# Kernel tuning notes

Hardware: AMD Instinct MI355X
Metric: run time of the kernel (lower is better)

Reference implementation:

```python
import jax, jax.numpy as jnp
import numpy as np

N_HEADS = 16
N_KV_HEADS = 4
N_EMBED = 2048
HEAD_DIM = 128
SECTIONS = [16, 24, 24, 16, 24, 24]


def _process_rotary(c):
    # c: [3, B, T, HEAD_DIM] -> [B, 1, T, HEAD_DIM]
    splits = np.cumsum(SECTIONS)[:-1]
    secs = jnp.split(c, splits, axis=-1)
    out = jnp.concatenate([s[i % 3] for i, s in enumerate(secs)], axis=-1)
    return out[:, None]  # add head axis


def _rotate_half(x):
    x1, x2 = jnp.split(x, 2, axis=-1)
    return jnp.concatenate([-x2, x1], axis=-1)


def setup_inputs() -> dict:
    key = jax.random.key(0)
    ks = jax.random.split(key, 12)
    B, T = 1, 2048
    s = 0.02
    return {
        "x": jax.random.normal(ks[0], (B, T, N_EMBED), jnp.float32),
        "cos": jax.random.uniform(ks[1], (3, B, T, HEAD_DIM), jnp.float32),
        "sin": jax.random.uniform(ks[2], (3, B, T, HEAD_DIM), jnp.float32),
        "Wq": jax.random.normal(ks[3], (N_EMBED, N_EMBED), jnp.float32) * s,
        "bq": jax.random.normal(ks[4], (N_EMBED,), jnp.float32) * s,
        "Wk": jax.random.normal(ks[5], (N_EMBED, N_KV_HEADS * HEAD_DIM), jnp.float32) * s,
        "bk": jax.random.normal(ks[6], (N_KV_HEADS * HEAD_DIM,), jnp.float32) * s,
        "Wv": jax.random.normal(ks[7], (N_EMBED, N_KV_HEADS * HEAD_DIM), jnp.float32) * s,
        "bv": jax.random.normal(ks[8], (N_KV_HEADS * HEAD_DIM,), jnp.float32) * s,
        "Wo": jax.random.normal(ks[9], (N_EMBED, N_EMBED), jnp.float32) * s,
    }


def reference(x, cos, sin, Wq, bq, Wk, bk, Wv, bv, Wo):
    B, T, C = x.shape
    H, Hkv, D = N_HEADS, N_KV_HEADS, HEAD_DIM
    q = (x @ Wq + bq).reshape(B, T, H, D).transpose(0, 2, 1, 3)    # [B,H,T,D]
    k = (x @ Wk + bk).reshape(B, T, Hkv, D).transpose(0, 2, 1, 3)  # [B,Hkv,T,D]
    v = (x @ Wv + bv).reshape(B, T, Hkv, D).transpose(0, 2, 1, 3)
    # multi-section rope (cos/sin are 4-dim -> custom path)
    c = _process_rotary(cos)
    s = _process_rotary(sin)
    q = q * c + _rotate_half(q) * s
    k = k * c + _rotate_half(k) * s
    present_k, present_v = k, v
    # GQA expansion (repeat_interleave over head axis)
    r = H // Hkv
    k = jnp.repeat(k, r, axis=1)
    v = jnp.repeat(v, r, axis=1)
    # causal SDPA
    scores = jnp.einsum("bhqd,bhkd->bhqk", q, k) / jnp.sqrt(jnp.float32(D))
    causal = jnp.tril(jnp.ones((T, T), dtype=bool))
    scores = jnp.where(causal, scores, jnp.finfo(scores.dtype).min)
    attn = jax.nn.softmax(scores, axis=-1)
    y = jnp.einsum("bhqk,bhkd->bhqd", attn, v)
    y = y.transpose(0, 2, 1, 3).reshape(B, T, C)
    y = y @ Wo
    return (y, present_k, present_v)
```

## Files before the change

kernel.cpp:

```cpp
#include <hip/hip_runtime.h>

typedef unsigned short u16;
typedef unsigned int u32;
typedef __attribute__((ext_vector_type(4))) float f32x4;
typedef __attribute__((ext_vector_type(8))) __bf16 bf16x8;
typedef __attribute__((ext_vector_type(4))) u16 u16x4;
typedef __attribute__((ext_vector_type(2))) u32 u32x2;


__device__ __forceinline__ u16 f2bf(float f) {
  union { float f; unsigned u; } v; v.f = f;
  unsigned r = v.u + 0x7fffu + ((v.u >> 16) & 1u);
  return (u16)(r >> 16);
}

__device__ __forceinline__ u32 pack_bf2(float a, float b) {
  union { float f; unsigned u; } x, y;
  x.f = a; y.f = b;
#if __has_builtin(__builtin_amdgcn_perm)
  return __builtin_amdgcn_perm(y.u + 0x8000u, x.u + 0x8000u, 0x07060302u);
#else
  return (u32)((x.u + 0x8000u) >> 16) | ((y.u + 0x8000u) & 0xffff0000u);
#endif
}

__device__ __forceinline__ void stage16(const void* g, void* l) {
#if __has_builtin(__builtin_amdgcn_global_load_lds)
  __builtin_amdgcn_global_load_lds((const __attribute__((address_space(1))) void*)g,
                                   (__attribute__((address_space(3))) void*)l, 16, 0, 0);
#else
  *(f32x4*)l = *(const f32x4*)g;
#endif
}

__device__ __forceinline__ f32x4 mfma16(bf16x8 a, bf16x8 b, f32x4 c) {
  return __builtin_amdgcn_mfma_f32_16x16x32_bf16(a, b, c, 0, 0, 0);
}

__device__ __forceinline__ float fexp2(float x) {
#if __has_builtin(__builtin_amdgcn_exp2f)
  return __builtin_amdgcn_exp2f(x);
#else
  return exp2f(x);
#endif
}

__device__ __forceinline__ int rope_ch(int d) {
  int dd = (d < 64) ? d : d - 64;
  return (dd < 16) ? 0 : (dd < 40 ? 1 : 2);
}


__global__ void yuna_convert_bf16(const float* __restrict__ in, u16* __restrict__ out, int n4) {
  int i = blockIdx.x * blockDim.x + threadIdx.x;
  if (i < n4) {
    f32x4 v = ((const f32x4*)in)[i];
    u16x4 o;
    o.x = f2bf(v.x); o.y = f2bf(v.y); o.z = f2bf(v.z); o.w = f2bf(v.w);
    ((u16x4*)out)[i] = o;
  }
}

__global__ void yuna_prep_weights(const float* __restrict__ Wq, const float* __restrict__ Wk,
                                  const float* __restrict__ Wv, const float* __restrict__ Wo,
                                  u16* __restrict__ Wb, u16* __restrict__ Wob) {
  __shared__ float tile[64][65];
  const int mat = blockIdx.z;
  const float* W;
  u16* out;
  int N;
  if (mat == 0)      { W = Wq; out = Wb;                          N = 2048; }
  else if (mat == 1) { W = Wk; out = Wb + (size_t)2048 * 2048;    N = 512; }
  else if (mat == 2) { W = Wv; out = Wb + (size_t)2560 * 2048;    N = 512; }
  else               { W = Wo; out = Wob;                         N = 2048; }
  int k0 = blockIdx.x * 64, n0 = blockIdx.y * 64;
  if (n0 >= N) return;
  int tx = threadIdx.x & 63, ty = threadIdx.x >> 6;
#pragma unroll
  for (int j = 0; j < 64; j += 4)
    tile[ty + j][tx] = W[(size_t)(k0 + ty + j) * N + n0 + tx];
  __syncthreads();
#pragma unroll
  for (int j = 0; j < 64; j += 4)
    out[(size_t)(n0 + ty + j) * 2048 + k0 + tx] = f2bf(tile[tx][ty + j]);
}

__global__ void yuna_transpose_v(const float* __restrict__ pv, u16* __restrict__ vtb) {
  __shared__ float tile[64][65];
  int t0 = blockIdx.x * 64, d0 = blockIdx.y * 64, kvh = blockIdx.z;
  int tx = threadIdx.x & 63, ty = threadIdx.x >> 6;
#pragma unroll
  for (int j = 0; j < 64; j += 4)
    tile[ty + j][tx] = pv[(size_t)(kvh * 2048 + t0 + ty + j) * 128 + d0 + tx];
  __syncthreads();
#pragma unroll
  for (int j = 0; j < 64; j += 4)
    vtb[(size_t)(kvh * 128 + d0 + ty + j) * 2048 + t0 + tx] = f2bf(tile[tx][ty + j]);
}

template <int WN>
__global__ __launch_bounds__(256, 2) void yuna_gemm_bt(
    const u16* __restrict__ A, const u16* __restrict__ Bt,
    float* __restrict__ C, int M, int N, int K) {
  constexpr int NF = WN / 16;
  constexpr int BROWS = 2 * WN;
  __shared__ __align__(16) u16 As[128 * 64];
  __shared__ __align__(16) u16 Bs[BROWS * 64];
  const int tid = threadIdx.x;
  const int wave = tid >> 6, lane = tid & 63;
  const int m0 = blockIdx.x * 128, n0 = blockIdx.y * (2 * WN);
  const int wr = (wave >> 1) * 64, wc = (wave & 1) * WN;
  const int lrow = lane & 15, lkg = lane >> 4;

  const int srow = tid >> 3;
  const int ssc = (tid & 7) ^ ((tid >> 3) & 7);
  const size_t abase = (size_t)(m0 + srow) * K + ssc * 8;
  const size_t bbase = (size_t)(n0 + srow) * K + ssc * 8;

  const f32x4 fzero = {0.f, 0.f, 0.f, 0.f};
  f32x4 acc[4][NF];
#pragma unroll
  for (int mi = 0; mi < 4; ++mi)
#pragma unroll
    for (int ni = 0; ni < NF; ++ni) acc[mi][ni] = fzero;

  const int sw = lrow & 7;
  for (int k0 = 0; k0 < K; k0 += 64) {
    __syncthreads();
#pragma unroll
    for (int it = 0; it < 4; ++it)
      stage16(A + abase + (size_t)it * 32 * K + k0, (char*)As + (tid + it * 256) * 16);
#pragma unroll
    for (int it = 0; it < BROWS / 32; ++it)
      stage16(Bt + bbase + (size_t)it * 32 * K + k0, (char*)Bs + (tid + it * 256) * 16);
    asm volatile("s_waitcnt vmcnt(0)" ::: "memory");
    __syncthreads();
#pragma unroll
    for (int kk = 0; kk < 2; ++kk) {
      const int cof = ((kk * 4 + lkg) ^ sw) << 4;
      bf16x8 af[4], bfr[NF];
#pragma unroll
      for (int mi = 0; mi < 4; ++mi)
        af[mi] = *(const bf16x8*)((const char*)As + (wr + mi * 16 + lrow) * 128 + cof);
#pragma unroll
      for (int ni = 0; ni < NF; ++ni)
        bfr[ni] = *(const bf16x8*)((const char*)Bs + (wc + ni * 16 + lrow) * 128 + cof);
#pragma unroll
      for (int mi = 0; mi < 4; ++mi)
#pragma unroll
        for (int ni = 0; ni < NF; ++ni)
          acc[mi][ni] = mfma16(af[mi], bfr[ni], acc[mi][ni]);
    }
  }
#pragma unroll
  for (int mi = 0; mi < 4; ++mi)
#pragma unroll
    for (int ni = 0; ni < NF; ++ni) {
      int r0 = m0 + wr + mi * 16 + lkg * 4;
      int c = n0 + wc + ni * 16 + lrow;
#pragma unroll
      for (int r = 0; r < 4; ++r)
        C[(size_t)(r0 + r) * N + c] = acc[mi][ni][r];
    }
}

__global__ void yuna_rope_scatter(
    const float* __restrict__ qkv, const float* __restrict__ bq,
    const float* __restrict__ bk, const float* __restrict__ bv,
    const float* __restrict__ cosp, const float* __restrict__ sinp,
    u16* __restrict__ qb, u16* __restrict__ kb,
    float* __restrict__ pk, float* __restrict__ pv) {
  const float QSCALE = 1.4426950408889634f * 0.08838834764831845f;
  int t = blockIdx.x;
  int tid = threadIdx.x;
  const float* row = qkv + (size_t)t * 3072;
  size_t cbase = (size_t)t * 128;
  for (int i = tid; i < 1024; i += 256) {
    int h = i >> 6, d = i & 63;
    float a = row[h * 128 + d] + bq[h * 128 + d];
    float b = row[h * 128 + d + 64] + bq[h * 128 + d + 64];
    float c0 = cosp[(size_t)rope_ch(d) * 262144 + cbase + d];
    float s0 = sinp[(size_t)rope_ch(d) * 262144 + cbase + d];
    float c1 = cosp[(size_t)rope_ch(d + 64) * 262144 + cbase + d + 64];
    float s1 = sinp[(size_t)rope_ch(d + 64) * 262144 + cbase + d + 64];
    float o0 = a * c0 - b * s0;
    float o1 = b * c1 + a * s1;
    size_t o = ((size_t)h * 2048 + t) * 128 + d;
    qb[o] = f2bf(o0 * QSCALE);
    qb[o + 64] = f2bf(o1 * QSCALE);
  }
  {
    int kvh = tid >> 6, d = tid & 63;
    float a = row[2048 + kvh * 128 + d] + bk[kvh * 128 + d];
    float b = row[2048 + kvh * 128 + d + 64] + bk[kvh * 128 + d + 64];
    float c0 = cosp[(size_t)rope_ch(d) * 262144 + cbase + d];
    float s0 = sinp[(size_t)rope_ch(d) * 262144 + cbase + d];
    float c1 = cosp[(size_t)rope_ch(d + 64) * 262144 + cbase + d + 64];
    float s1 = sinp[(size_t)rope_ch(d + 64) * 262144 + cbase + d + 64];
    float o0 = a * c0 - b * s0;
    float o1 = b * c1 + a * s1;
    size_t o = ((size_t)kvh * 2048 + t) * 128 + d;
    kb[o] = f2bf(o0); kb[o + 64] = f2bf(o1);
    pk[o] = o0; pk[o + 64] = o1;
  }
  for (int i = tid; i < 512; i += 256) {
    int kvh = i >> 7, d = i & 127;
    pv[((size_t)kvh * 2048 + t) * 128 + d] = row[2560 + kvh * 128 + d] + bv[kvh * 128 + d];
  }
}

__global__ __launch_bounds__(256, 2) void yuna_flash_attn(
    const u16* __restrict__ Q,
    const u16* __restrict__ Kb,
    const u16* __restrict__ Vt,
    u16* __restrict__ Y) {
  __shared__ __align__(16) u16 Ks[2][64 * 128];
  __shared__ __align__(16) u16 Vs[2][128 * 64];
  __shared__ __align__(16) u16 Ps[64 * 64];
  const int h = blockIdx.x;
  const int yb = blockIdx.y;
  const int qb = (yb < 16) ? yb : 47 - yb;
  const int kvh = h >> 2;
  const int tid = threadIdx.x, wave = tid >> 6, lane = tid & 63;
  const int lrow = lane & 15, lkg = lane >> 4;
  const int m = wave * 16 + lrow;
  const int sw = lrow & 7;

  const int krow = tid >> 4;
  const int ksc = (tid & 15) ^ ((tid >> 4) & 7);
  const size_t kbase0 = ((size_t)(kvh * 2048 + krow) << 7) + ksc * 8;
  const int vrow = tid >> 3;
  const int vsc = (tid & 7) ^ ((tid >> 3) & 7);
  const size_t vbase0 = (size_t)(kvh * 128 + vrow) * 2048 + vsc * 8;

  bf16x8 qf[4];
#pragma unroll
  for (int kk = 0; kk < 4; ++kk)
    qf[kk] = *(const bf16x8*)(Q + (((size_t)h * 2048 + qb * 64 + m) << 7) + kk * 32 + lkg * 8);

  const f32x4 fzero = {0.f, 0.f, 0.f, 0.f};
  f32x4 o[8];
#pragma unroll
  for (int dt = 0; dt < 8; ++dt) o[dt] = fzero;
  float m_i = -1e30f, l_i = 0.f;

  const int nkb = qb + 1;

#pragma unroll
  for (int it = 0; it < 4; ++it)
    stage16(Kb + kbase0 + ((size_t)(it * 16) << 7), (char*)Ks[0] + (tid + it * 256) * 16);
#pragma unroll
  for (int it = 0; it < 4; ++it)
    stage16(Vt + vbase0 + (size_t)it * 32 * 2048, (char*)Vs[0] + (tid + it * 256) * 16);

  for (int kb = 0; kb < nkb; ++kb) {
    const int cur = kb & 1;
    const char* Ksb = (const char*)Ks[cur];
    const char* Vsb = (const char*)Vs[cur];
    if (kb + 1 < nkb) {
      char* Ksn = (char*)Ks[cur ^ 1];
      char* Vsn = (char*)Vs[cur ^ 1];
#pragma unroll
      for (int it = 0; it < 4; ++it)
        stage16(Kb + kbase0 + ((size_t)((kb + 1) * 64 + it * 16) << 7), Ksn + (tid + it * 256) * 16);
#pragma unroll
      for (int it = 0; it < 4; ++it)
        stage16(Vt + vbase0 + (size_t)it * 32 * 2048 + (kb + 1) * 64, Vsn + (tid + it * 256) * 16);
      asm volatile("s_waitcnt vmcnt(8)\n\ts_barrier" ::: "memory");
    } else {
      asm volatile("s_waitcnt vmcnt(0)\n\ts_barrier" ::: "memory");
    }

    f32x4 s[4];
#pragma unroll
    for (int nt = 0; nt < 4; ++nt) s[nt] = fzero;
#pragma unroll
    for (int kk = 0; kk < 4; ++kk) {
      const int cof = ((kk * 4 + lkg) ^ sw) << 4;
      bf16x8 kf[4];
#pragma unroll
      for (int nt = 0; nt < 4; ++nt)
        kf[nt] = *(const bf16x8*)(Ksb + (nt * 16 + lrow) * 256 + cof);
#pragma unroll
      for (int nt = 0; nt < 4; ++nt)
        s[nt] = mfma16(kf[nt], qf[kk], s[nt]);
    }
    if (kb == qb) {
#pragma unroll
      for (int nt = 0; nt < 4; ++nt)
#pragma unroll
        for (int r = 0; r < 4; ++r)
          if (nt * 16 + lkg * 4 + r > m) s[nt][r] = -1e30f;
    }

    float mx = -1e30f;
#pragma unroll
    for (int nt = 0; nt < 4; ++nt)
#pragma unroll
      for (int r = 0; r < 4; ++r) mx = fmaxf(mx, s[nt][r]);
    mx = fmaxf(mx, __shfl_xor(mx, 16));
    mx = fmaxf(mx, __shfl_xor(mx, 32));
    float mnew = fmaxf(m_i, mx);
    float alpha = fexp2(m_i - mnew);
    m_i = mnew;
    float ps = 0.f;
    const int hh = lkg & 1;
#pragma unroll
    for (int nt = 0; nt < 4; ++nt) {
      float p0 = fexp2(s[nt][0] - mnew);
      float p1 = fexp2(s[nt][1] - mnew);
      float p2 = fexp2(s[nt][2] - mnew);
      float p3 = fexp2(s[nt][3] - mnew);
      ps += (p0 + p1) + (p2 + p3);
      u32x2 pk2;
      pk2.x = pack_bf2(p0, p1);
      pk2.y = pack_bf2(p2, p3);
      int cc = 2 * nt + (lkg >> 1);
      *(u32x2*)((char*)Ps + m * 128 + ((cc ^ (m & 7)) << 4) + hh * 8) = pk2;
    }
    ps += __shfl_xor(ps, 16);
    ps += __shfl_xor(ps, 32);
    l_i = l_i * alpha + ps;
#pragma unroll
    for (int dt = 0; dt < 8; ++dt) o[dt] *= alpha;

#pragma unroll
    for (int kk = 0; kk < 2; ++kk) {
      const int cof = ((kk * 4 + lkg) ^ sw) << 4;
      bf16x8 pf = *(const bf16x8*)((char*)Ps + m * 128 + cof);
      bf16x8 vf[8];
#pragma unroll
      for (int dt = 0; dt < 8; ++dt)
        vf[dt] = *(const bf16x8*)(Vsb + (dt * 16 + lrow) * 128 + cof);
#pragma unroll
      for (int dt = 0; dt < 8; ++dt)
        o[dt] = mfma16(vf[dt], pf, o[dt]);
    }
    asm volatile("s_barrier" ::: "memory");
  }

  __syncthreads();
  {
    float inv = 1.f / l_i;
    const int hh = lkg & 1;
#pragma unroll
    for (int dt = 0; dt < 8; ++dt) {
      u32x2 w2;
      w2.x = pack_bf2(o[dt][0] * inv, o[dt][1] * inv);
      w2.y = pack_bf2(o[dt][2] * inv, o[dt][3] * inv);
      int cc = 2 * dt + (lkg >> 1);
      *(u32x2*)((char*)Ks[0] + m * 256 + ((cc ^ (m & 7)) << 4) + hh * 8) = w2;
    }
  }
  __syncthreads();
#pragma unroll
  for (int it = 0; it < 4; ++it) {
    int c = tid + it * 256;
    int row = c >> 4, cc = c & 15;
    f32x4 v = *(const f32x4*)((const char*)Ks[0] + row * 256 + ((cc ^ (row & 7)) << 4));
    *(f32x4*)(Y + (size_t)(qb * 64 + row) * 2048 + h * 128 + cc * 8) = v;
  }
}


extern "C" void kernel_launch(void* const* d_in, const int* in_sizes, int n_in,
                              void* d_out, int out_size, void* d_ws, size_t ws_size,
                              hipStream_t stream) {
  const float* x = (const float*)d_in[0];
  const float* cosp = (const float*)d_in[1];
  const float* sinp = (const float*)d_in[2];
  const float* Wq = (const float*)d_in[3];
  const float* bq = (const float*)d_in[4];
  const float* Wk = (const float*)d_in[5];
  const float* bk = (const float*)d_in[6];
  const float* Wv = (const float*)d_in[7];
  const float* bv = (const float*)d_in[8];
  const float* Wo = (const float*)d_in[9];
  float* out = (float*)d_out;
  float* out_k = out + 4194304;
  float* out_v = out + 5242880;

  char* ws = (char*)d_ws;
  u16* xb   = (u16*)(ws + 0);
  u16* Wb   = (u16*)(ws + 8388608);
  u16* Wob  = (u16*)(ws + 20971520);
  float* qkv = (float*)(ws + 29360128);
  u16* qbuf = (u16*)(ws + 54525952);
  u16* kbuf = (u16*)(ws + 62914560);
  u16* vtb  = (u16*)(ws + 65011712);
  u16* yat  = (u16*)(ws + 67108864);

  yuna_convert_bf16<<<4096, 256, 0, stream>>>(x, xb, 1048576);
  yuna_prep_weights<<<dim3(32, 32, 4), 256, 0, stream>>>(Wq, Wk, Wv, Wo, Wb, Wob);
  yuna_gemm_bt<48><<<dim3(16, 32), 256, 0, stream>>>(xb, Wb, qkv, 2048, 3072, 2048);
  yuna_rope_scatter<<<2048, 256, 0, stream>>>(qkv, bq, bk, bv, cosp, sinp,
                                              qbuf, kbuf, out_k, out_v);
  yuna_transpose_v<<<dim3(32, 2, 4), 256, 0, stream>>>(out_v, vtb);
  yuna_flash_attn<<<dim3(16, 32), 256, 0, stream>>>(qbuf, kbuf, vtb, yat);
  yuna_gemm_bt<32><<<dim3(16, 32), 256, 0, stream>>>(yat, Wob, out, 2048, 2048, 2048);
}
```

Before: 242.2 us.

## Fuse bias, RoPE and V transpose into QKV GEMM epilogue with double-buffered tiles

The QKV GEMM now writes bf16 Q/K, the fp32 present K/V and the transposed bf16 V directly from its epilogue. It applies bias and RoPE there using cos/sin tables pre-selected per section in the convert kernel. This removes the fp32 qkv intermediate plus the separate rope_scatter and transpose_v kernels. Both GEMMs switch to 64x128 tiles with double-buffered LDS staging and occupancy 3, trading larger grids for overlap of loads with MFMA. The epilogue writes are scattered 2-byte stores, which may be less coalesced.

```diff
diff --git a/kernel.cpp b/kernel.cpp
--- a/kernel.cpp
+++ b/kernel.cpp
@@ -51,13 +51,29 @@
 }
 
 
-__global__ void yuna_convert_bf16(const float* __restrict__ in, u16* __restrict__ out, int n4) {
-  int i = blockIdx.x * blockDim.x + threadIdx.x;
-  if (i < n4) {
+__global__ void yuna_convert_prep(const float* __restrict__ in, u16* __restrict__ out,
+                                  const float* __restrict__ cosp, const float* __restrict__ sinp,
+                                  float* __restrict__ csel, float* __restrict__ ssel) {
+  int b = blockIdx.x;
+  if (b < 4096) {
+    int i = b * 256 + threadIdx.x;
     f32x4 v = ((const f32x4*)in)[i];
     u16x4 o;
     o.x = f2bf(v.x); o.y = f2bf(v.y); o.z = f2bf(v.z); o.w = f2bf(v.w);
     ((u16x4*)out)[i] = o;
+  } else {
+    int i = (b - 4096) * 256 + threadIdx.x;
+    int i4 = i * 4;
+    int t = i4 >> 7, d = i4 & 127;
+    f32x4 c, s;
+#pragma unroll
+    for (int j = 0; j < 4; ++j) {
+      int ch = rope_ch(d + j);
+      c[j] = cosp[(size_t)ch * 262144 + (size_t)t * 128 + d + j];
+      s[j] = sinp[(size_t)ch * 262144 + (size_t)t * 128 + d + j];
+    }
+    ((f32x4*)csel)[i] = c;
+    ((f32x4*)ssel)[i] = s;
   }
 }
 
@@ -85,32 +101,21 @@
     out[(size_t)(n0 + ty + j) * 2048 + k0 + tx] = f2bf(tile[tx][ty + j]);
 }
 
-__global__ void yuna_transpose_v(const float* __restrict__ pv, u16* __restrict__ vtb) {
-  __shared__ float tile[64][65];
-  int t0 = blockIdx.x * 64, d0 = blockIdx.y * 64, kvh = blockIdx.z;
-  int tx = threadIdx.x & 63, ty = threadIdx.x >> 6;
-#pragma unroll
-  for (int j = 0; j < 64; j += 4)
-    tile[ty + j][tx] = pv[(size_t)(kvh * 2048 + t0 + ty + j) * 128 + d0 + tx];
-  __syncthreads();
-#pragma unroll
-  for (int j = 0; j < 64; j += 4)
-    vtb[(size_t)(kvh * 128 + d0 + ty + j) * 2048 + t0 + tx] = f2bf(tile[tx][ty + j]);
-}
-
-template <int WN>
-__global__ __launch_bounds__(256, 2) void yuna_gemm_bt(
+__global__ __launch_bounds__(256, 3) void yuna_gemm_qkv(
     const u16* __restrict__ A, const u16* __restrict__ Bt,
-    float* __restrict__ C, int M, int N, int K) {
-  constexpr int NF = WN / 16;
-  constexpr int BROWS = 2 * WN;
-  __shared__ __align__(16) u16 As[128 * 64];
-  __shared__ __align__(16) u16 Bs[BROWS * 64];
+    const float* __restrict__ bq, const float* __restrict__ bk, const float* __restrict__ bv,
+    const float* __restrict__ csel, const float* __restrict__ ssel,
+    u16* __restrict__ qb, u16* __restrict__ kb, u16* __restrict__ vtb,
+    float* __restrict__ pk, float* __restrict__ pv) {
+  const int K = 2048;
+  __shared__ __align__(16) char smem[49152];
   const int tid = threadIdx.x;
   const int wave = tid >> 6, lane = tid & 63;
-  const int m0 = blockIdx.x * 128, n0 = blockIdx.y * (2 * WN);
-  const int wr = (wave >> 1) * 64, wc = (wave & 1) * WN;
   const int lrow = lane & 15, lkg = lane >> 4;
+  const int m0 = blockIdx.x * 64;
+  const int by = blockIdx.y;
+  const int n0 = by * 128;
+  const int sw = lrow & 7;
 
   const int srow = tid >> 3;
   const int ssc = (tid & 7) ^ ((tid >> 3) & 7);
@@ -118,95 +123,179 @@
   const size_t bbase = (size_t)(n0 + srow) * K + ssc * 8;
 
   const f32x4 fzero = {0.f, 0.f, 0.f, 0.f};
-  f32x4 acc[4][NF];
-#pragma unroll
-  for (int mi = 0; mi < 4; ++mi)
-#pragma unroll
-    for (int ni = 0; ni < NF; ++ni) acc[mi][ni] = fzero;
-
-  const int sw = lrow & 7;
-  for (int k0 = 0; k0 < K; k0 += 64) {
-    __syncthreads();
-#pragma unroll
-    for (int it = 0; it < 4; ++it)
-      stage16(A + abase + (size_t)it * 32 * K + k0, (char*)As + (tid + it * 256) * 16);
-#pragma unroll
-    for (int it = 0; it < BROWS / 32; ++it)
-      stage16(Bt + bbase + (size_t)it * 32 * K + k0, (char*)Bs + (tid + it * 256) * 16);
-    asm volatile("s_waitcnt vmcnt(0)" ::: "memory");
-    __syncthreads();
+  f32x4 acc[4][2];
+#pragma unroll
+  for (int mi = 0; mi < 4; ++mi) { acc[mi][0] = fzero; acc[mi][1] = fzero; }
+
+#pragma unroll
+  for (int it = 0; it < 2; ++it)
+    stage16(A + abase + (size_t)it * 32 * K, smem + (tid + it * 256) * 16);
+#pragma unroll
+  for (int it = 0; it < 4; ++it)
+    stage16(Bt + bbase + (size_t)it * 32 * K, smem + 16384 + (tid + it * 256) * 16);
+
+  for (int k0 = 0, ki = 0; k0 < K; k0 += 64, ++ki) {
+    const int cur = ki & 1;
+    const char* Asb = smem + cur * 8192;
+    const char* Bsb = smem + 16384 + cur * 16384;
+    if (k0 + 64 < K) {
+      char* Asn = smem + (cur ^ 1) * 8192;
+      char* Bsn = smem + 16384 + (cur ^ 1) * 16384;
+#pragma unroll
+      for (int it = 0; it < 2; ++it)
+        stage16(A + abase + (size_t)it * 32 * K + k0 + 64, Asn + (tid + it * 256) * 16);
+#pragma unroll
+      for (int it = 0; it < 4; ++it)
+        stage16(Bt + bbase + (size_t)it * 32 * K + k0 + 64, Bsn + (tid + it * 256) * 16);
+      asm volatile("s_waitcnt vmcnt(6)\n\ts_barrier" ::: "memory");
+    } else {
+      asm volatile("s_waitcnt vmcnt(0)\n\ts_barrier" ::: "memory");
+    }
 #pragma unroll
     for (int kk = 0; kk < 2; ++kk) {
       const int cof = ((kk * 4 + lkg) ^ sw) << 4;
-      bf16x8 af[4], bfr[NF];
+      bf16x8 af[4], bfr[2];
 #pragma unroll
       for (int mi = 0; mi < 4; ++mi)
-        af[mi] = *(const bf16x8*)((const char*)As + (wr + mi * 16 + lrow) * 128 + cof);
-#pragma unroll
-      for (int ni = 0; ni < NF; ++ni)
-        bfr[ni] = *(const bf16x8*)((const char*)Bs + (wc + ni * 16 + lrow) * 128 + cof);
+        af[mi] = *(const bf16x8*)(Asb + (mi * 16 + lrow) * 128 + cof);
+#pragma unroll
+      for (int ni = 0; ni < 2; ++ni)
+        bfr[ni] = *(const bf16x8*)(Bsb + (wave * 16 + ni * 64 + lrow) * 128 + cof);
 #pragma unroll
       for (int mi = 0; mi < 4; ++mi)
 #pragma unroll
-        for (int ni = 0; ni < NF; ++ni)
+        for (int ni = 0; ni < 2; ++ni)
           acc[mi][ni] = mfma16(af[mi], bfr[ni], acc[mi][ni]);
     }
+    asm volatile("s_barrier" ::: "memory");
+  }
+
+  if (by >= 20) {
+    const int kvh = by - 20;
+#pragma unroll
+    for (int mi = 0; mi < 4; ++mi)
+#pragma unroll
+      for (int ni = 0; ni < 2; ++ni) {
+        int d = wave * 16 + ni * 64 + lrow;
+        float bb = bv[kvh * 128 + d];
+        int mb = mi * 16 + lkg * 4;
+        float v0 = acc[mi][ni][0] + bb, v1 = acc[mi][ni][1] + bb;
+        float v2 = acc[mi][ni][2] + bb, v3 = acc[mi][ni][3] + bb;
+        size_t pb = ((size_t)(kvh * 2048 + m0 + mb)) * 128 + d;
+        pv[pb] = v0; pv[pb + 128] = v1; pv[pb + 256] = v2; pv[pb + 384] = v3;
+        u16x4 w;
+        w.x = f2bf(v0); w.y = f2bf(v1); w.z = f2bf(v2); w.w = f2bf(v3);
+        *(u16x4*)(vtb + ((size_t)(kvh * 128 + d)) * 2048 + m0 + mb) = w;
+      }
+  } else {
+    const float QSCALE = 1.4426950408889634f * 0.08838834764831845f;
+    const bool isQ = (by < 16);
+    const int h = isQ ? by : (by - 16);
+    const float* bias = isQ ? bq : bk;
+    const int dlo = wave * 16 + lrow;
+    const float blo = bias[h * 128 + dlo];
+    const float bhi = bias[h * 128 + dlo + 64];
+#pragma unroll
+    for (int mi = 0; mi < 4; ++mi) {
+      const int tb = m0 + mi * 16 + lkg * 4;
+#pragma unroll
+      for (int r = 0; r < 4; ++r) {
+        const int t = tb + r;
+        float a = acc[mi][0][r] + blo;
+        float b = acc[mi][1][r] + bhi;
+        size_t cb = (size_t)t * 128 + dlo;
+        float cl = csel[cb], sl = ssel[cb];
+        float ch = csel[cb + 64], sh = ssel[cb + 64];
+        float lo = a * cl - b * sl;
+        float hi = b * ch + a * sh;
+        size_t o = (((size_t)(h * 2048 + t)) << 7) + dlo;
+        if (isQ) {
+          qb[o] = f2bf(lo * QSCALE);
+          qb[o + 64] = f2bf(hi * QSCALE);
+        } else {
+          kb[o] = f2bf(lo);
+          kb[o + 64] = f2bf(hi);
+          pk[o] = lo; pk[o + 64] = hi;
+        }
+      }
+    }
+  }
+}
+
+__global__ __launch_bounds__(256, 3) void yuna_gemm_out(
+    const u16* __restrict__ A, const u16* __restrict__ Bt, float* __restrict__ C) {
+  const int K = 2048;
+  __shared__ __align__(16) char smem[49152];
+  const int tid = threadIdx.x;
+  const int wave = tid >> 6, lane = tid & 63;
+  const int lrow = lane & 15, lkg = lane >> 4;
+  const int m0 = blockIdx.x * 64;
+  const int n0 = blockIdx.y * 128;
+  const int wc = wave * 32;
+  const int sw = lrow & 7;
+
+  const int srow = tid >> 3;
+  const int ssc = (tid & 7) ^ ((tid >> 3) & 7);
+  const size_t abase = (size_t)(m0 + srow) * K + ssc * 8;
+  const size_t bbase = (size_t)(n0 + srow) * K + ssc * 8;
+
+  const f32x4 fzero = {0.f, 0.f, 0.f, 0.f};
+  f32x4 acc[4][2];
+#pragma unroll
+  for (int mi = 0; mi < 4; ++mi) { acc[mi][0] = fzero; acc[mi][1] = fzero; }
+
+#pragma unroll
+  for (int it = 0; it < 2; ++it)
+    stage16(A + abase + (size_t)it * 32 * K, smem + (tid + it * 256) * 16);
+#pragma unroll
+  for (int it = 0; it < 4; ++it)
+    stage16(Bt + bbase + (size_t)it * 32 * K, smem + 16384 + (tid + it * 256) * 16);
+
+  for (int k0 = 0, ki = 0; k0 < K; k0 += 64, ++ki) {
+    const int cur = ki & 1;
+    const char* Asb = smem + cur * 8192;
+    const char* Bsb = smem + 16384 + cur * 16384;
+    if (k0 + 64 < K) {
+      char* Asn = smem + (cur ^ 1) * 8192;
+      char* Bsn = smem + 16384 + (cur ^ 1) * 16384;
+#pragma unroll
+      for (int it = 0; it < 2; ++it)
+        stage16(A + abase + (size_t)it * 32 * K + k0 + 64, Asn + (tid + it * 256) * 16);
+#pragma unroll
+      for (int it = 0; it < 4; ++it)
+        stage16(Bt + bbase + (size_t)it * 32 * K + k0 + 64, Bsn + (tid + it * 256) * 16);
+      asm volatile("s_waitcnt vmcnt(6)\n\ts_barrier" ::: "memory");
+    } else {
+      asm volatile("s_waitcnt vmcnt(0)\n\ts_barrier" ::: "memory");
+    }
+#pragma unroll
+    for (int kk = 0; kk < 2; ++kk) {
+      const int cof = ((kk * 4 + lkg) ^ sw) << 4;
+      bf16x8 af[4], bfr[2];
+#pragma unroll
+      for (int mi = 0; mi < 4; ++mi)
+        af[mi] = *(const bf16x8*)(Asb + (mi * 16 + lrow) * 128 + cof);
+#pragma unroll
+      for (int ni = 0; ni < 2; ++ni)
+        bfr[ni] = *(const bf16x8*)(Bsb + (wc + ni * 16 + lrow) * 128 + cof);
+#pragma unroll
+      for (int mi = 0; mi < 4; ++mi)
+#pragma unroll
+        for (int ni = 0; ni < 2; ++ni)
+          acc[mi][ni] = mfma16(af[mi], bfr[ni], acc[mi][ni]);
+    }
+    asm volatile("s_barrier" ::: "memory");
   }
 #pragma unroll
   for (int mi = 0; mi < 4; ++mi)
 #pragma unroll
-    for (int ni = 0; ni < NF; ++ni) {
-      int r0 = m0 + wr + mi * 16 + lkg * 4;
-      int c = n0 + wc + ni * 16 + lrow;
+    for (int ni = 0; ni < 2; ++ni) {
+      int d = wc + ni * 16 + lrow;
+      int mb = mi * 16 + lkg * 4;
 #pragma unroll
       for (int r = 0; r < 4; ++r)
-        C[(size_t)(r0 + r) * N + c] = acc[mi][ni][r];
-    }
-}
-
-__global__ void yuna_rope_scatter(
-    const float* __restrict__ qkv, const float* __restrict__ bq,
-    const float* __restrict__ bk, const float* __restrict__ bv,
-    const float* __restrict__ cosp, const float* __restrict__ sinp,
-    u16* __restrict__ qb, u16* __restrict__ kb,
-    float* __restrict__ pk, float* __restrict__ pv) {
-  const float QSCALE = 1.4426950408889634f * 0.08838834764831845f;
-  int t = blockIdx.x;
-  int tid = threadIdx.x;
-  const float* row = qkv + (size_t)t * 3072;
-  size_t cbase = (size_t)t * 128;
-  for (int i = tid; i < 1024; i += 256) {
-    int h = i >> 6, d = i & 63;
-    float a = row[h * 128 + d] + bq[h * 128 + d];
-    float b = row[h * 128 + d + 64] + bq[h * 128 + d + 64];
-    float c0 = cosp[(size_t)rope_ch(d) * 262144 + cbase + d];
-    float s0 = sinp[(size_t)rope_ch(d) * 262144 + cbase + d];
-    float c1 = cosp[(size_t)rope_ch(d + 64) * 262144 + cbase + d + 64];
-    float s1 = sinp[(size_t)rope_ch(d + 64) * 262144 + cbase + d + 64];
-    float o0 = a * c0 - b * s0;
-    float o1 = b * c1 + a * s1;
-    size_t o = ((size_t)h * 2048 + t) * 128 + d;
-    qb[o] = f2bf(o0 * QSCALE);
-    qb[o + 64] = f2bf(o1 * QSCALE);
-  }
-  {
-    int kvh = tid >> 6, d = tid & 63;
-    float a = row[2048 + kvh * 128 + d] + bk[kvh * 128 + d];
-    float b = row[2048 + kvh * 128 + d + 64] + bk[kvh * 128 + d + 64];
-    float c0 = cosp[(size_t)rope_ch(d) * 262144 + cbase + d];
-    float s0 = sinp[(size_t)rope_ch(d) * 262144 + cbase + d];
-    float c1 = cosp[(size_t)rope_ch(d + 64) * 262144 + cbase + d + 64];
-    float s1 = sinp[(size_t)rope_ch(d + 64) * 262144 + cbase + d + 64];
-    float o0 = a * c0 - b * s0;
-    float o1 = b * c1 + a * s1;
-    size_t o = ((size_t)kvh * 2048 + t) * 128 + d;
-    kb[o] = f2bf(o0); kb[o + 64] = f2bf(o1);
-    pk[o] = o0; pk[o + 64] = o1;
-  }
-  for (int i = tid; i < 512; i += 256) {
-    int kvh = i >> 7, d = i & 127;
-    pv[((size_t)kvh * 2048 + t) * 128 + d] = row[2560 + kvh * 128 + d] + bv[kvh * 128 + d];
-  }
+        C[(size_t)(m0 + mb + r) * 2048 + n0 + d] = acc[mi][ni][r];
+    }
 }
 
 __global__ __launch_bounds__(256, 2) void yuna_flash_attn(
@@ -384,18 +473,17 @@
   u16* xb   = (u16*)(ws + 0);
   u16* Wb   = (u16*)(ws + 8388608);
   u16* Wob  = (u16*)(ws + 20971520);
-  float* qkv = (float*)(ws + 29360128);
+  float* csel = (float*)(ws + 29360128);
+  float* ssel = (float*)(ws + 30408704);
   u16* qbuf = (u16*)(ws + 54525952);
   u16* kbuf = (u16*)(ws + 62914560);
   u16* vtb  = (u16*)(ws + 65011712);
   u16* yat  = (u16*)(ws + 67108864);
 
-  yuna_convert_bf16<<<4096, 256, 0, stream>>>(x, xb, 1048576);
+  yuna_convert_prep<<<4352, 256, 0, stream>>>(x, xb, cosp, sinp, csel, ssel);
   yuna_prep_weights<<<dim3(32, 32, 4), 256, 0, stream>>>(Wq, Wk, Wv, Wo, Wb, Wob);
-  yuna_gemm_bt<48><<<dim3(16, 32), 256, 0, stream>>>(xb, Wb, qkv, 2048, 3072, 2048);
-  yuna_rope_scatter<<<2048, 256, 0, stream>>>(qkv, bq, bk, bv, cosp, sinp,
-                                              qbuf, kbuf, out_k, out_v);
-  yuna_transpose_v<<<dim3(32, 2, 4), 256, 0, stream>>>(out_v, vtb);
+  yuna_gemm_qkv<<<dim3(32, 24), 256, 0, stream>>>(xb, Wb, bq, bk, bv, csel, ssel,
+                                                  qbuf, kbuf, vtb, out_k, out_v);
   yuna_flash_attn<<<dim3(16, 32), 256, 0, stream>>>(qbuf, kbuf, vtb, yat);
-  yuna_gemm_bt<32><<<dim3(16, 32), 256, 0, stream>>>(yat, Wob, out, 2048, 2048, 2048);
-}
+  yuna_gemm_out<<<dim3(32, 16), 256, 0, stream>>>(yat, Wob, out);
+}
```

Result: faster. 227.0 us (-6.3%).
